# Optimization experiments

Measured on AMD Instinct MI355X. Metric: run time of the kernel, lower is better.

Reference implementation:

```python
import jax, jax.numpy as jnp
import numpy as np

NSX, NSY = 8, 8          # subdomain grid
BATCH = 8                # PDE instances
PTS = 100_000            # points per instance
IN_C, HID, OUT_C = 32, 64, 32
NUM_CLUSTERS = BATCH * NSX * NSY  # 512


def _clusters(coords, batch_ids):
    # coords assumed in [0,1]^2; bucket into NSX x NSY grid per batch sample
    ix = jnp.clip((coords[:, 0] * NSX).astype(jnp.int32), 0, NSX - 1)
    iy = jnp.clip((coords[:, 1] * NSY).astype(jnp.int32), 0, NSY - 1)
    return batch_ids * (NSX * NSY) + iy * NSX + ix


def _mlp(h, W1, b1, W2, b2):
    # Linear -> GELU(exact, matches torch nn.GELU default) -> Linear
    return jax.nn.gelu(h @ W1 + b1, approximate=False) @ W2 + b2


def setup_inputs() -> dict:
    key = jax.random.key(0)
    ks = jax.random.split(key, 12)
    N = BATCH * PTS
    x = jax.random.normal(ks[0], (N, IN_C), dtype=jnp.float32)
    src_coords = jax.random.uniform(ks[1], (N, 2), dtype=jnp.float32)
    tgt_coords = jax.random.uniform(ks[2], (N, 2), dtype=jnp.float32)
    src_batch = jnp.repeat(jnp.arange(BATCH, dtype=jnp.int32), PTS)
    tgt_batch = jnp.repeat(jnp.arange(BATCH, dtype=jnp.int32), PTS)
    def lin(k, fan_in, fan_out):
        s = 1.0 / np.sqrt(fan_in)
        kw, kb = jax.random.split(k)
        W = jax.random.uniform(kw, (fan_in, fan_out), minval=-s, maxval=s, dtype=jnp.float32)
        b = jax.random.uniform(kb, (fan_out,), minval=-s, maxval=s, dtype=jnp.float32)
        return W, b
    Wv1, bv1 = lin(ks[3], IN_C, HID)
    Wv2, bv2 = lin(ks[4], HID, HID)
    Wt1, bt1 = lin(ks[5], 2 + HID, HID)
    Wt2, bt2 = lin(ks[6], HID, OUT_C)
    return {"x": x, "src_coords": src_coords, "src_batch": src_batch,
            "tgt_coords": tgt_coords, "tgt_batch": tgt_batch,
            "Wv1": Wv1, "bv1": bv1, "Wv2": Wv2, "bv2": bv2,
            "Wt1": Wt1, "bt1": bt1, "Wt2": Wt2, "bt2": bt2}


def reference(x, src_coords, src_batch, tgt_coords, tgt_batch,
              Wv1, bv1, Wv2, bv2, Wt1, bt1, Wt2, bt2):
    src_cl = _clusters(src_coords, src_batch)        # [Ns]
    tgt_cl = _clusters(tgt_coords, tgt_batch)        # [Nt]
    h = _mlp(x, Wv1, bv1, Wv2, bv2)                  # [Ns, HID]
    # subdomain mean-pool (the integral over each subdomain)
    s = jax.ops.segment_sum(h, src_cl, num_segments=NUM_CLUSTERS)        # [C, HID]
    cnt = jax.ops.segment_sum(jnp.ones((h.shape[0], 1), h.dtype), src_cl,
                              num_segments=NUM_CLUSTERS)                 # [C, 1]
    pooled = s / jnp.maximum(cnt, 1.0)
    # broadcast pooled feature to each target point, concat target coords
    feat = jnp.concatenate([tgt_coords, pooled[tgt_cl]], axis=-1)        # [Nt, 2+HID]
    return _mlp(feat, Wt1, bt1, Wt2, bt2)            # [Nt, OUT_C]
```

## Files before the change

### kernel.cpp

```cpp
#include <hip/hip_runtime.h>

#define NC   512
#define INC  32
#define HID  64
#define OUTC 32
#define STRZ 68
#define GSTR 36

typedef __attribute__((ext_vector_type(8))) __bf16 bf16x8;
typedef __attribute__((ext_vector_type(4))) float  f32x4;
typedef __attribute__((ext_vector_type(8))) float  f32x8;
typedef __attribute__((ext_vector_type(8))) unsigned int   u32x8;
typedef __attribute__((ext_vector_type(8))) unsigned short u16x8;
typedef __attribute__((ext_vector_type(4))) unsigned short u16x4;

static __device__ __forceinline__ f32x4 mfma16(bf16x8 a, bf16x8 b, f32x4 c){
    return __builtin_amdgcn_mfma_f32_16x16x32_bf16(a, b, c, 0, 0, 0);
}

__device__ __forceinline__ float gelu_f(float v){
    const float s  = v * 0.70710678118654752f;
    const float as = fabsf(s);
    const float t  = __builtin_amdgcn_rcpf(__builtin_fmaf(0.3275911f, as, 1.0f));
    const float e  = __expf(-as * as);
    float p = __builtin_fmaf(1.061405429f, t, -1.453152027f);
    p = __builtin_fmaf(p, t, 1.421413741f);
    p = __builtin_fmaf(p, t, -0.284496736f);
    p = __builtin_fmaf(p, t, 0.254829592f);
    p = p * t;
    float er = __builtin_fmaf(-p, e, 1.0f);
    er = copysignf(er, s);
    return 0.5f * v * (1.0f + er);
}

__device__ __forceinline__ void split8v(f32x8 x, bf16x8& hi, bf16x8& lo){
    u32x8 ux = __builtin_bit_cast(u32x8, x);
    f32x8 hf = __builtin_bit_cast(f32x8, ux & 0xFFFF0000u);
    f32x8 lf = x - hf;
    u32x8 ul = __builtin_bit_cast(u32x8, lf);
    hi = __builtin_bit_cast(bf16x8, __builtin_convertvector(ux >> 16, u16x8));
    lo = __builtin_bit_cast(bf16x8, __builtin_convertvector(ul >> 16, u16x8));
}

__device__ __forceinline__ unsigned short rneb(float f){
    unsigned int u = __float_as_uint(f);
    u += 0x7FFFu + ((u >> 16) & 1u);
    return (unsigned short)(u >> 16);
}

__global__ __launch_bounds__(256, 3) void k_src(
    const float* __restrict__ x, const float* __restrict__ sc,
    const float* __restrict__ Wv1, const float* __restrict__ bv1,
    float* __restrict__ partial, float* __restrict__ pcntf,
    int npb, int T, int bpb)
{
    __shared__ ushort gbuf[2][4][64][GSTR];
    __shared__ ushort lcw[2][4][32];
    const int t = threadIdx.x;
    const int wave = t >> 6, lane = t & 63;
    const int lrow = lane & 15, lgrp = lane >> 4;
    const int batch = blockIdx.x / bpb;
    const int pb    = blockIdx.x % bpb;

    bf16x8 Bh0, Bh1, Bh2, Bh3, Bl0, Bl1, Bl2, Bl3;
    float bnt0, bnt1, bnt2, bnt3;
    {
        f32x8 w;
        #pragma unroll
        for (int j = 0; j < 8; j++) w[j] = Wv1[(8*lgrp + j)*HID +  0 + lrow];
        split8v(w, Bh0, Bl0);  bnt0 = bv1[ 0 + lrow];
        #pragma unroll
        for (int j = 0; j < 8; j++) w[j] = Wv1[(8*lgrp + j)*HID + 16 + lrow];
        split8v(w, Bh1, Bl1);  bnt1 = bv1[16 + lrow];
        #pragma unroll
        for (int j = 0; j < 8; j++) w[j] = Wv1[(8*lgrp + j)*HID + 32 + lrow];
        split8v(w, Bh2, Bl2);  bnt2 = bv1[32 + lrow];
        #pragma unroll
        for (int j = 0; j < 8; j++) w[j] = Wv1[(8*lgrp + j)*HID + 48 + lrow];
        split8v(w, Bh3, Bl3);  bnt3 = bv1[48 + lrow];
    }
    u16x8 onesu;
    #pragma unroll
    for (int j = 0; j < 8; j++) onesu[j] = 0x3F80u;
    const bf16x8 ONE = __builtin_bit_cast(bf16x8, onesu);

    f32x4 P0 = (f32x4){0.f,0.f,0.f,0.f}, P1 = P0, P2 = P0, P3 = P0, C = P0;

    const int base   = batch * npb + pb * T * 16;
    const int PAIRS  = T >> 1;
    const int rounds = (PAIRS + 3) >> 2;

    int  p_cur  = wave;
    bool a_cur  = p_cur < PAIRS;
    float2 sA_c, sB_c; f32x8 xA_c, xB_c;
    if (a_cur){
        const int pt0 = base + p_cur * 32;
        sA_c = ((const float2*)sc)[pt0 + lrow];
        sB_c = ((const float2*)sc)[pt0 + 16 + lrow];
        xA_c = *(const f32x8*)(x + (size_t)(pt0 + lrow)*INC + 8*lgrp);
        xB_c = *(const f32x8*)(x + (size_t)(pt0 + 16 + lrow)*INC + 8*lgrp);
    }

    for (int r = 0; r < rounds; r++){
        const int buf = r & 1;
        const int  p_nxt = p_cur + 4;
        const bool a_nxt = p_nxt < PAIRS;
        float2 sA_n, sB_n; f32x8 xA_n, xB_n;
        if (a_nxt){
            const int pt0 = base + p_nxt * 32;
            sA_n = ((const float2*)sc)[pt0 + lrow];
            sB_n = ((const float2*)sc)[pt0 + 16 + lrow];
            xA_n = *(const f32x8*)(x + (size_t)(pt0 + lrow)*INC + 8*lgrp);
            xB_n = *(const f32x8*)(x + (size_t)(pt0 + 16 + lrow)*INC + 8*lgrp);
        }

        if (a_cur){
            int ixA = (int)(sA_c.x * 8.0f); ixA = ixA < 0 ? 0 : (ixA > 7 ? 7 : ixA);
            int iyA = (int)(sA_c.y * 8.0f); iyA = iyA < 0 ? 0 : (iyA > 7 ? 7 : iyA);
            int ixB = (int)(sB_c.x * 8.0f); ixB = ixB < 0 ? 0 : (ixB > 7 ? 7 : ixB);
            int iyB = (int)(sB_c.y * 8.0f); iyB = iyB < 0 ? 0 : (iyB > 7 ? 7 : iyB);
            if (lgrp == 0){
                lcw[buf][wave][lrow]      = (ushort)((iyA << 3) + ixA);
                lcw[buf][wave][16 + lrow] = (ushort)((iyB << 3) + ixB);
            }
            {
                bf16x8 Ah = __builtin_convertvector(xA_c, bf16x8);
                f32x4 a0 = (f32x4){0.f,0.f,0.f,0.f}, a1 = a0, a2 = a0, a3 = a0;
                a0 = mfma16(Ah, Bl0, a0); a1 = mfma16(Ah, Bl1, a1);
                a2 = mfma16(Ah, Bl2, a2); a3 = mfma16(Ah, Bl3, a3);
                a0 = mfma16(Ah, Bh0, a0); a1 = mfma16(Ah, Bh1, a1);
                a2 = mfma16(Ah, Bh2, a2); a3 = mfma16(Ah, Bh3, a3);
                u16x4 w4;
                w4[0]=rneb(gelu_f(a0[0]+bnt0)); w4[1]=rneb(gelu_f(a0[1]+bnt0));
                w4[2]=rneb(gelu_f(a0[2]+bnt0)); w4[3]=rneb(gelu_f(a0[3]+bnt0));
                *(u16x4*)&gbuf[buf][wave][ 0 + lrow][4*lgrp] = w4;
                w4[0]=rneb(gelu_f(a1[0]+bnt1)); w4[1]=rneb(gelu_f(a1[1]+bnt1));
                w4[2]=rneb(gelu_f(a1[2]+bnt1)); w4[3]=rneb(gelu_f(a1[3]+bnt1));
                *(u16x4*)&gbuf[buf][wave][16 + lrow][4*lgrp] = w4;
                w4[0]=rneb(gelu_f(a2[0]+bnt2)); w4[1]=rneb(gelu_f(a2[1]+bnt2));
                w4[2]=rneb(gelu_f(a2[2]+bnt2)); w4[3]=rneb(gelu_f(a2[3]+bnt2));
                *(u16x4*)&gbuf[buf][wave][32 + lrow][4*lgrp] = w4;
                w4[0]=rneb(gelu_f(a3[0]+bnt3)); w4[1]=rneb(gelu_f(a3[1]+bnt3));
                w4[2]=rneb(gelu_f(a3[2]+bnt3)); w4[3]=rneb(gelu_f(a3[3]+bnt3));
                *(u16x4*)&gbuf[buf][wave][48 + lrow][4*lgrp] = w4;
            }
            {
                bf16x8 Ah = __builtin_convertvector(xB_c, bf16x8);
                f32x4 a0 = (f32x4){0.f,0.f,0.f,0.f}, a1 = a0, a2 = a0, a3 = a0;
                a0 = mfma16(Ah, Bl0, a0); a1 = mfma16(Ah, Bl1, a1);
                a2 = mfma16(Ah, Bl2, a2); a3 = mfma16(Ah, Bl3, a3);
                a0 = mfma16(Ah, Bh0, a0); a1 = mfma16(Ah, Bh1, a1);
                a2 = mfma16(Ah, Bh2, a2); a3 = mfma16(Ah, Bh3, a3);
                u16x4 w4;
                w4[0]=rneb(gelu_f(a0[0]+bnt0)); w4[1]=rneb(gelu_f(a0[1]+bnt0));
                w4[2]=rneb(gelu_f(a0[2]+bnt0)); w4[3]=rneb(gelu_f(a0[3]+bnt0));
                *(u16x4*)&gbuf[buf][wave][ 0 + lrow][16 + 4*lgrp] = w4;
                w4[0]=rneb(gelu_f(a1[0]+bnt1)); w4[1]=rneb(gelu_f(a1[1]+bnt1));
                w4[2]=rneb(gelu_f(a1[2]+bnt1)); w4[3]=rneb(gelu_f(a1[3]+bnt1));
                *(u16x4*)&gbuf[buf][wave][16 + lrow][16 + 4*lgrp] = w4;
                w4[0]=rneb(gelu_f(a2[0]+bnt2)); w4[1]=rneb(gelu_f(a2[1]+bnt2));
                w4[2]=rneb(gelu_f(a2[2]+bnt2)); w4[3]=rneb(gelu_f(a2[3]+bnt2));
                *(u16x4*)&gbuf[buf][wave][32 + lrow][16 + 4*lgrp] = w4;
                w4[0]=rneb(gelu_f(a3[0]+bnt3)); w4[1]=rneb(gelu_f(a3[1]+bnt3));
                w4[2]=rneb(gelu_f(a3[2]+bnt3)); w4[3]=rneb(gelu_f(a3[3]+bnt3));
                *(u16x4*)&gbuf[buf][wave][48 + lrow][16 + 4*lgrp] = w4;
            }
        } else {
            if (lgrp == 0){
                lcw[buf][wave][lrow]      = 0xFFFFu;
                lcw[buf][wave][16 + lrow] = 0xFFFFu;
            }
            u16x4 zz = (u16x4){0,0,0,0};
            #pragma unroll
            for (int nt = 0; nt < 4; nt++){
                *(u16x4*)&gbuf[buf][wave][16*nt + lrow][4*lgrp] = zz;
                *(u16x4*)&gbuf[buf][wave][16*nt + lrow][16 + 4*lgrp] = zz;
            }
        }
        __syncthreads();

        const ushort tgt = (ushort)(16*wave + lrow);
        #pragma unroll
        for (int s = 0; s < 4; s++){
            const u16x8 lcv = *(const u16x8*)&lcw[buf][s][8*lgrp];
            u16x8 ohu;
            #pragma unroll
            for (int j = 0; j < 8; j++)
                ohu[j] = (lcv[j] == tgt) ? (ushort)0x3F80u : (ushort)0;
            const bf16x8 oh = __builtin_bit_cast(bf16x8, ohu);
            u16x4 glo, ghi;
            glo = *(const u16x4*)&gbuf[buf][s][ 0 + lrow][8*lgrp];
            ghi = *(const u16x4*)&gbuf[buf][s][ 0 + lrow][8*lgrp + 4];
            bf16x8 g0 = __builtin_bit_cast(bf16x8, __builtin_shufflevector(glo, ghi, 0,1,2,3,4,5,6,7));
            glo = *(const u16x4*)&gbuf[buf][s][16 + lrow][8*lgrp];
            ghi = *(const u16x4*)&gbuf[buf][s][16 + lrow][8*lgrp + 4];
            bf16x8 g1 = __builtin_bit_cast(bf16x8, __builtin_shufflevector(glo, ghi, 0,1,2,3,4,5,6,7));
            glo = *(const u16x4*)&gbuf[buf][s][32 + lrow][8*lgrp];
            ghi = *(const u16x4*)&gbuf[buf][s][32 + lrow][8*lgrp + 4];
            bf16x8 g2 = __builtin_bit_cast(bf16x8, __builtin_shufflevector(glo, ghi, 0,1,2,3,4,5,6,7));
            glo = *(const u16x4*)&gbuf[buf][s][48 + lrow][8*lgrp];
            ghi = *(const u16x4*)&gbuf[buf][s][48 + lrow][8*lgrp + 4];
            bf16x8 g3 = __builtin_bit_cast(bf16x8, __builtin_shufflevector(glo, ghi, 0,1,2,3,4,5,6,7));
            P0 = mfma16(oh, g0, P0);
            P1 = mfma16(oh, g1, P1);
            P2 = mfma16(oh, g2, P2);
            P3 = mfma16(oh, g3, P3);
            C  = mfma16(oh, ONE, C);
        }

        p_cur = p_nxt; a_cur = a_nxt;
        sA_c = sA_n; sB_c = sB_n; xA_c = xA_n; xB_c = xB_n;
    }

    float* dst = partial + (size_t)blockIdx.x * 4096;
    #pragma unroll
    for (int reg = 0; reg < 4; reg++){
        const int row = 16*wave + 4*lgrp + reg;
        dst[row*64 +  0 + lrow] = P0[reg];
        dst[row*64 + 16 + lrow] = P1[reg];
        dst[row*64 + 32 + lrow] = P2[reg];
        dst[row*64 + 48 + lrow] = P3[reg];
    }
    if (lrow == 0){
        #pragma unroll
        for (int reg = 0; reg < 4; reg++)
            pcntf[(size_t)blockIdx.x*64 + 16*wave + 4*lgrp + reg] = C[reg];
    }
}

__global__ __launch_bounds__(256) void k_cluster(
    const float* __restrict__ partial, const float* __restrict__ pcntf,
    const float* __restrict__ Wv2, const float* __restrict__ bv2,
    const float* __restrict__ Wt1, const float* __restrict__ bt1,
    float* __restrict__ z, int spb)
{
    __shared__ float red[4][HID];
    __shared__ float redn[4];
    __shared__ float m[HID];
    __shared__ float ph[HID];
    const int c = blockIdx.x;
    const int t = threadIdx.x, j = t & 63, sl = t >> 6;
    const int batch = c >> 6, lc = c & 63;

    float s = 0.0f, cn = 0.0f;
    for (int b = sl; b < spb; b += 4){
        const size_t slot = (size_t)batch * spb + b;
        s  += partial[slot * 4096 + (size_t)lc * 64 + j];
        cn += pcntf[slot * 64 + lc];
    }
    red[sl][j] = s;
    if (j == 0) redn[sl] = cn;
    __syncthreads();

    if (sl == 0){
        float stot = red[0][j] + red[1][j] + red[2][j] + red[3][j];
        float ntot = redn[0] + redn[1] + redn[2] + redn[3];
        const float inv = (ntot > 0.0f) ? (1.0f / ntot) : 0.0f;
        m[j] = stot * inv;
        __builtin_amdgcn_s_barrier();
        float a = bv2[j];
        #pragma unroll 8
        for (int i = 0; i < HID; i++) a += m[i] * Wv2[i*HID + j];
        if (ntot <= 0.0f) a = 0.0f;
        ph[j] = a;
        __builtin_amdgcn_s_barrier();
        float b = bt1[j];
        #pragma unroll 8
        for (int i = 0; i < HID; i++) b += ph[i] * Wt1[(2 + i)*HID + j];
        z[c*HID + j] = b;
    }
}

__global__ __launch_bounds__(256, 3) void k_tgt(
    const float* __restrict__ tc,
    const float* __restrict__ z, const float* __restrict__ Wt1,
    const float* __restrict__ Wt2, const float* __restrict__ bt2,
    float* __restrict__ out, int npb, int TT, int bpt)
{
    __shared__ float zs[64*STRZ];
    const int t = threadIdx.x;
    const int wave = t >> 6, lane = t & 63;
    const int lrow = lane & 15, lgrp = lane >> 4;
    const int batch = blockIdx.x / bpt;
    const int toff  = (blockIdx.x % bpt) * TT;

    for (int k = t; k < 4096; k += 256)
        zs[(k >> 6)*STRZ + (k & 63)] = z[(size_t)(batch*64)*HID + k];

    bf16x8 Bh00, Bh01, Bh10, Bh11, Bl00, Bl01, Bl10, Bl11;
    f32x8 w0v0, w0v1, w1v0, w1v1;
    {
        f32x8 w;
        #pragma unroll
        for (int j = 0; j < 8; j++) w[j] = Wt2[( 0 + 8*lgrp + j)*OUTC +  0 + lrow];
        split8v(w, Bh00, Bl00);
        #pragma unroll
        for (int j = 0; j < 8; j++) w[j] = Wt2[( 0 + 8*lgrp + j)*OUTC + 16 + lrow];
        split8v(w, Bh01, Bl01);
        #pragma unroll
        for (int j = 0; j < 8; j++) w[j] = Wt2[(32 + 8*lgrp + j)*OUTC +  0 + lrow];
        split8v(w, Bh10, Bl10);
        #pragma unroll
        for (int j = 0; j < 8; j++) w[j] = Wt2[(32 + 8*lgrp + j)*OUTC + 16 + lrow];
        split8v(w, Bh11, Bl11);
        #pragma unroll
        for (int j = 0; j < 8; j++){
            w0v0[j] = Wt1[ 0 + 8*lgrp + j];
            w0v1[j] = Wt1[32 + 8*lgrp + j];
            w1v0[j] = Wt1[HID +  0 + 8*lgrp + j];
            w1v1[j] = Wt1[HID + 32 + 8*lgrp + j];
        }
    }
    const float bo0 = bt2[lrow], bo1 = bt2[16 + lrow];
    __syncthreads();

    const size_t pbase = (size_t)batch * npb;
    float2 c2_c = ((const float2*)tc)[pbase + (size_t)(toff + wave)*16 + lrow];

    for (int tt = toff + wave; tt < toff + TT; tt += 4){
        const int ttn = tt + 4;
        float2 c2_n = c2_c;
        if (ttn < toff + TT)
            c2_n = ((const float2*)tc)[pbase + (size_t)ttn*16 + lrow];

        int ix = (int)(c2_c.x * 8.0f); ix = ix < 0 ? 0 : (ix > 7 ? 7 : ix);
        int iy = (int)(c2_c.y * 8.0f); iy = iy < 0 ? 0 : (iy > 7 ? 7 : iy);
        const int zb = ((iy << 3) + ix) * STRZ;

        f32x8 z0 = *(const f32x8*)(&zs[zb +  0 + 8*lgrp]);
        f32x8 z1 = *(const f32x8*)(&zs[zb + 32 + 8*lgrp]);
        f32x8 g0, g1;
        #pragma unroll
        for (int j = 0; j < 8; j++){
            g0[j] = gelu_f(z0[j] + c2_c.x * w0v0[j] + c2_c.y * w1v0[j]);
            g1[j] = gelu_f(z1[j] + c2_c.x * w0v1[j] + c2_c.y * w1v1[j]);
        }
        bf16x8 Ah0, Al0, Ah1, Al1;
        split8v(g0, Ah0, Al0);
        split8v(g1, Ah1, Al1);

        f32x4 a0 = (f32x4){0.f,0.f,0.f,0.f}, a1 = a0;
        a0 = mfma16(Al0, Bh00, a0); a1 = mfma16(Al0, Bh01, a1);
        a0 = mfma16(Ah0, Bl00, a0); a1 = mfma16(Ah0, Bl01, a1);
        a0 = mfma16(Ah0, Bh00, a0); a1 = mfma16(Ah0, Bh01, a1);
        a0 = mfma16(Al1, Bh10, a0); a1 = mfma16(Al1, Bh11, a1);
        a0 = mfma16(Ah1, Bl10, a0); a1 = mfma16(Ah1, Bl11, a1);
        a0 = mfma16(Ah1, Bh10, a0); a1 = mfma16(Ah1, Bh11, a1);

        const size_t prow = pbase + (size_t)tt*16 + 4*lgrp;
        #pragma unroll
        for (int q = 0; q < 4; q++){
            out[(prow + q)*OUTC +  0 + lrow] = a0[q] + bo0;
            out[(prow + q)*OUTC + 16 + lrow] = a1[q] + bo1;
        }
        c2_c = c2_n;
    }
}

extern "C" void kernel_launch(void* const* d_in, const int* in_sizes, int n_in,
                              void* d_out, int out_size, void* d_ws, size_t ws_size,
                              hipStream_t stream)
{
    const float* x   = (const float*)d_in[0];
    const float* sc  = (const float*)d_in[1];
    const int*   sb  = (const int*)  d_in[2];  (void)sb;
    const float* tc  = (const float*)d_in[3];
    const int*   tb  = (const int*)  d_in[4];  (void)tb;
    const float* Wv1 = (const float*)d_in[5];
    const float* bv1 = (const float*)d_in[6];
    const float* Wv2 = (const float*)d_in[7];
    const float* bv2 = (const float*)d_in[8];
    const float* Wt1 = (const float*)d_in[9];
    const float* bt1 = (const float*)d_in[10];
    const float* Wt2 = (const float*)d_in[11];
    const float* bt2 = (const float*)d_in[12];
    float* out = (float*)d_out;

    const int n   = in_sizes[2];
    const int npb = n / 8;
    const int tiles_pb = npb / 16;

    int bpb = 1;
    const int cands[4] = {125, 25, 5, 1};
    for (int ci = 0; ci < 4; ci++){
        const int d = cands[ci];
        if (tiles_pb % d) continue;
        if ((tiles_pb / d) & 1) continue;
        const size_t slots = (size_t)8 * d;
        const size_t need  = slots * 4096 * 4 + slots * 64 * 4 + (size_t)NC*HID*4 + 4096;
        if (need <= ws_size){ bpb = d; break; }
    }
    const int T    = tiles_pb / bpb;
    const int nblk = 8 * bpb;
    const size_t slots = (size_t)nblk;

    char* ws = (char*)d_ws;
    float* partial = (float*)(ws);
    float* pcntf   = (float*)(ws + slots * 4096 * 4);
    float* z       = (float*)(ws + slots * 4096 * 4 + slots * 64 * 4);

    k_src    <<<nblk, 256, 0, stream>>>(x, sc, Wv1, bv1, partial, pcntf, npb, T, bpb);
    k_cluster<<<NC, 256, 0, stream>>>(partial, pcntf, Wv2, bv2, Wt1, bt1, z, bpb);

    int TT = 1;
    const int tcands[5] = {25, 10, 5, 2, 1};
    for (int ci = 0; ci < 5; ci++){
        if (tiles_pb % tcands[ci] == 0){ TT = tcands[ci]; break; }
    }
    const int bpt = tiles_pb / TT;
    k_tgt    <<<8*bpt, 256, 0, stream>>>(tc, z, Wt1, Wt2, bt2, out, npb, TT, bpt);
}
```

Baseline: 105.6 us.

## Use cheaper erf approximation, hardware bf16 pack, LDS-transposed output stores, smaller target tiles

Replaces the 5-term Abramowitz-Stegun erf polynomial in GELU with a lower-order 3-term variant, which cuts ALU work but loses accuracy. The manual round-to-nearest bf16 packing is swapped for a vector convert that should map to hardware pack instructions. The target kernel now stages MFMA results through a per-wave LDS transpose so each row is written with 16-byte vector stores instead of scattered scalar stores. The target tile preference changes from 25 to 10 tiles per block, giving more blocks.

```diff
diff --git a/kernel.cpp b/kernel.cpp
--- a/kernel.cpp
+++ b/kernel.cpp
@@ -6,8 +6,10 @@
 #define OUTC 32
 #define STRZ 68
 #define GSTR 36
+#define TSTR 40
 
 typedef __attribute__((ext_vector_type(8))) __bf16 bf16x8;
+typedef __attribute__((ext_vector_type(4))) __bf16 bf16x4;
 typedef __attribute__((ext_vector_type(4))) float  f32x4;
 typedef __attribute__((ext_vector_type(8))) float  f32x8;
 typedef __attribute__((ext_vector_type(8))) unsigned int   u32x8;
@@ -21,12 +23,10 @@
 __device__ __forceinline__ float gelu_f(float v){
     const float s  = v * 0.70710678118654752f;
     const float as = fabsf(s);
-    const float t  = __builtin_amdgcn_rcpf(__builtin_fmaf(0.3275911f, as, 1.0f));
+    const float t  = __builtin_amdgcn_rcpf(__builtin_fmaf(0.47047f, as, 1.0f));
     const float e  = __expf(-as * as);
-    float p = __builtin_fmaf(1.061405429f, t, -1.453152027f);
-    p = __builtin_fmaf(p, t, 1.421413741f);
-    p = __builtin_fmaf(p, t, -0.284496736f);
-    p = __builtin_fmaf(p, t, 0.254829592f);
+    float p = __builtin_fmaf(0.7478556f, t, -0.0958798f);
+    p = __builtin_fmaf(p, t, 0.3480242f);
     p = p * t;
     float er = __builtin_fmaf(-p, e, 1.0f);
     er = copysignf(er, s);
@@ -42,10 +42,8 @@
     lo = __builtin_bit_cast(bf16x8, __builtin_convertvector(ul >> 16, u16x8));
 }
 
-__device__ __forceinline__ unsigned short rneb(float f){
-    unsigned int u = __float_as_uint(f);
-    u += 0x7FFFu + ((u >> 16) & 1u);
-    return (unsigned short)(u >> 16);
+__device__ __forceinline__ u16x4 pack4(f32x4 g){
+    return __builtin_bit_cast(u16x4, __builtin_convertvector(g, bf16x4));
 }
 
 __global__ __launch_bounds__(256, 3) void k_src(
@@ -130,19 +128,19 @@
                 a2 = mfma16(Ah, Bl2, a2); a3 = mfma16(Ah, Bl3, a3);
                 a0 = mfma16(Ah, Bh0, a0); a1 = mfma16(Ah, Bh1, a1);
                 a2 = mfma16(Ah, Bh2, a2); a3 = mfma16(Ah, Bh3, a3);
-                u16x4 w4;
-                w4[0]=rneb(gelu_f(a0[0]+bnt0)); w4[1]=rneb(gelu_f(a0[1]+bnt0));
-                w4[2]=rneb(gelu_f(a0[2]+bnt0)); w4[3]=rneb(gelu_f(a0[3]+bnt0));
-                *(u16x4*)&gbuf[buf][wave][ 0 + lrow][4*lgrp] = w4;
-                w4[0]=rneb(gelu_f(a1[0]+bnt1)); w4[1]=rneb(gelu_f(a1[1]+bnt1));
-                w4[2]=rneb(gelu_f(a1[2]+bnt1)); w4[3]=rneb(gelu_f(a1[3]+bnt1));
-                *(u16x4*)&gbuf[buf][wave][16 + lrow][4*lgrp] = w4;
-                w4[0]=rneb(gelu_f(a2[0]+bnt2)); w4[1]=rneb(gelu_f(a2[1]+bnt2));
-                w4[2]=rneb(gelu_f(a2[2]+bnt2)); w4[3]=rneb(gelu_f(a2[3]+bnt2));
-                *(u16x4*)&gbuf[buf][wave][32 + lrow][4*lgrp] = w4;
-                w4[0]=rneb(gelu_f(a3[0]+bnt3)); w4[1]=rneb(gelu_f(a3[1]+bnt3));
-                w4[2]=rneb(gelu_f(a3[2]+bnt3)); w4[3]=rneb(gelu_f(a3[3]+bnt3));
-                *(u16x4*)&gbuf[buf][wave][48 + lrow][4*lgrp] = w4;
+                f32x4 gv;
+                gv[0]=gelu_f(a0[0]+bnt0); gv[1]=gelu_f(a0[1]+bnt0);
+                gv[2]=gelu_f(a0[2]+bnt0); gv[3]=gelu_f(a0[3]+bnt0);
+                *(u16x4*)&gbuf[buf][wave][ 0 + lrow][4*lgrp] = pack4(gv);
+                gv[0]=gelu_f(a1[0]+bnt1); gv[1]=gelu_f(a1[1]+bnt1);
+                gv[2]=gelu_f(a1[2]+bnt1); gv[3]=gelu_f(a1[3]+bnt1);
+                *(u16x4*)&gbuf[buf][wave][16 + lrow][4*lgrp] = pack4(gv);
+                gv[0]=gelu_f(a2[0]+bnt2); gv[1]=gelu_f(a2[1]+bnt2);
+                gv[2]=gelu_f(a2[2]+bnt2); gv[3]=gelu_f(a2[3]+bnt2);
+                *(u16x4*)&gbuf[buf][wave][32 + lrow][4*lgrp] = pack4(gv);
+                gv[0]=gelu_f(a3[0]+bnt3); gv[1]=gelu_f(a3[1]+bnt3);
+                gv[2]=gelu_f(a3[2]+bnt3); gv[3]=gelu_f(a3[3]+bnt3);
+                *(u16x4*)&gbuf[buf][wave][48 + lrow][4*lgrp] = pack4(gv);
             }
             {
                 bf16x8 Ah = __builtin_convertvector(xB_c, bf16x8);
@@ -151,19 +149,19 @@
                 a2 = mfma16(Ah, Bl2, a2); a3 = mfma16(Ah, Bl3, a3);
                 a0 = mfma16(Ah, Bh0, a0); a1 = mfma16(Ah, Bh1, a1);
                 a2 = mfma16(Ah, Bh2, a2); a3 = mfma16(Ah, Bh3, a3);
-                u16x4 w4;
-                w4[0]=rneb(gelu_f(a0[0]+bnt0)); w4[1]=rneb(gelu_f(a0[1]+bnt0));
-                w4[2]=rneb(gelu_f(a0[2]+bnt0)); w4[3]=rneb(gelu_f(a0[3]+bnt0));
-                *(u16x4*)&gbuf[buf][wave][ 0 + lrow][16 + 4*lgrp] = w4;
-                w4[0]=rneb(gelu_f(a1[0]+bnt1)); w4[1]=rneb(gelu_f(a1[1]+bnt1));
-                w4[2]=rneb(gelu_f(a1[2]+bnt1)); w4[3]=rneb(gelu_f(a1[3]+bnt1));
-                *(u16x4*)&gbuf[buf][wave][16 + lrow][16 + 4*lgrp] = w4;
-                w4[0]=rneb(gelu_f(a2[0]+bnt2)); w4[1]=rneb(gelu_f(a2[1]+bnt2));
-                w4[2]=rneb(gelu_f(a2[2]+bnt2)); w4[3]=rneb(gelu_f(a2[3]+bnt2));
-                *(u16x4*)&gbuf[buf][wave][32 + lrow][16 + 4*lgrp] = w4;
-                w4[0]=rneb(gelu_f(a3[0]+bnt3)); w4[1]=rneb(gelu_f(a3[1]+bnt3));
-                w4[2]=rneb(gelu_f(a3[2]+bnt3)); w4[3]=rneb(gelu_f(a3[3]+bnt3));
-                *(u16x4*)&gbuf[buf][wave][48 + lrow][16 + 4*lgrp] = w4;
+                f32x4 gv;
+                gv[0]=gelu_f(a0[0]+bnt0); gv[1]=gelu_f(a0[1]+bnt0);
+                gv[2]=gelu_f(a0[2]+bnt0); gv[3]=gelu_f(a0[3]+bnt0);
+                *(u16x4*)&gbuf[buf][wave][ 0 + lrow][16 + 4*lgrp] = pack4(gv);
+                gv[0]=gelu_f(a1[0]+bnt1); gv[1]=gelu_f(a1[1]+bnt1);
+                gv[2]=gelu_f(a1[2]+bnt1); gv[3]=gelu_f(a1[3]+bnt1);
+                *(u16x4*)&gbuf[buf][wave][16 + lrow][16 + 4*lgrp] = pack4(gv);
+                gv[0]=gelu_f(a2[0]+bnt2); gv[1]=gelu_f(a2[1]+bnt2);
+                gv[2]=gelu_f(a2[2]+bnt2); gv[3]=gelu_f(a2[3]+bnt2);
+                *(u16x4*)&gbuf[buf][wave][32 + lrow][16 + 4*lgrp] = pack4(gv);
+                gv[0]=gelu_f(a3[0]+bnt3); gv[1]=gelu_f(a3[1]+bnt3);
+                gv[2]=gelu_f(a3[2]+bnt3); gv[3]=gelu_f(a3[3]+bnt3);
+                *(u16x4*)&gbuf[buf][wave][48 + lrow][16 + 4*lgrp] = pack4(gv);
             }
         } else {
             if (lgrp == 0){
@@ -278,6 +276,7 @@
     float* __restrict__ out, int npb, int TT, int bpt)
 {
     __shared__ float zs[64*STRZ];
+    __shared__ __align__(16) float trans[4][16][TSTR];
     const int t = threadIdx.x;
     const int wave = t >> 6, lane = t & 63;
     const int lrow = lane & 15, lgrp = lane >> 4;
@@ -316,6 +315,9 @@
 
     const size_t pbase = (size_t)batch * npb;
     float2 c2_c = ((const float2*)tc)[pbase + (size_t)(toff + wave)*16 + lrow];
+
+    const int rpt = lane >> 3;
+    const int rko = (lane & 7) * 4;
 
     for (int tt = toff + wave; tt < toff + TT; tt += 4){
         const int ttn = tt + 4;
@@ -347,12 +349,17 @@
         a0 = mfma16(Ah1, Bl10, a0); a1 = mfma16(Ah1, Bl11, a1);
         a0 = mfma16(Ah1, Bh10, a0); a1 = mfma16(Ah1, Bh11, a1);
 
-        const size_t prow = pbase + (size_t)tt*16 + 4*lgrp;
         #pragma unroll
         for (int q = 0; q < 4; q++){
-            out[(prow + q)*OUTC +  0 + lrow] = a0[q] + bo0;
-            out[(prow + q)*OUTC + 16 + lrow] = a1[q] + bo1;
-        }
+            trans[wave][4*lgrp + q][lrow]      = a0[q] + bo0;
+            trans[wave][4*lgrp + q][16 + lrow] = a1[q] + bo1;
+        }
+        const size_t prow = pbase + (size_t)tt*16;
+        f32x4 v0 = *(const f32x4*)&trans[wave][rpt][rko];
+        f32x4 v1 = *(const f32x4*)&trans[wave][8 + rpt][rko];
+        *(f32x4*)(out + (prow + rpt)*OUTC + rko)     = v0;
+        *(f32x4*)(out + (prow + 8 + rpt)*OUTC + rko) = v1;
+
         c2_c = c2_n;
     }
 }
@@ -403,7 +410,7 @@
     k_cluster<<<NC, 256, 0, stream>>>(partial, pcntf, Wv2, bv2, Wt1, bt1, z, bpb);
 
     int TT = 1;
-    const int tcands[5] = {25, 10, 5, 2, 1};
+    const int tcands[5] = {10, 25, 5, 2, 1};
     for (int ci = 0; ci < 5; ci++){
         if (tiles_pb % tcands[ci] == 0){ TT = tcands[ci]; break; }
     }
```

After: 104.2 us. No clear change (-1.3%).
